# Performance work log

Measured on AMD Instinct MI355X. Metric: run time of the kernel, lower is better.

Reference implementation:

```python
import jax, jax.numpy as jnp
import numpy as np

VOCAB = 1024   # must equal HID (embedding Linear consumes vocab-sized x)
HID = 1024
EMB = 256
NOS = 12
B, M = 512, 8
TEMP = 1.0


def setup_inputs() -> dict:
    key = jax.random.key(0)
    ks = jax.random.split(key, 12)
    N = B * M
    target = jax.random.normal(ks[0], (B, M, HID), jnp.float32)
    # precomputed standard Gumbel noise per step (training=True path)
    u = jax.random.uniform(ks[1], (NOS, N, VOCAB), jnp.float32, 1e-6, 1.0 - 1e-6)
    gumbels = -jnp.log(-jnp.log(u))
    sh = 1.0 / np.sqrt(HID)
    sv = 1.0 / np.sqrt(VOCAB)
    sos = 0.01 * jax.random.normal(ks[2], (EMB,), jnp.float32)
    W_ih = jax.random.uniform(ks[3], (HID, EMB), jnp.float32, -sh, sh)
    b_ih = jax.random.uniform(ks[4], (HID,), jnp.float32, -sh, sh)
    W_hh = jax.random.uniform(ks[5], (HID, HID), jnp.float32, -sh, sh)
    b_hh = jax.random.uniform(ks[6], (HID,), jnp.float32, -sh, sh)
    W_out = jax.random.uniform(ks[7], (VOCAB, HID), jnp.float32, -sh, sh)
    b_out = jax.random.uniform(ks[8], (VOCAB,), jnp.float32, -sh, sh)
    W_emb = jax.random.uniform(ks[9], (EMB, VOCAB), jnp.float32, -sv, sv)
    b_emb = jax.random.uniform(ks[10], (EMB,), jnp.float32, -sv, sv)
    return dict(target=target, gumbels=gumbels, sos=sos,
                W_ih=W_ih, b_ih=b_ih, W_hh=W_hh, b_hh=b_hh,
                W_out=W_out, b_out=b_out, W_emb=W_emb, b_emb=b_emb)


def reference(target, gumbels, sos, W_ih, b_ih, W_hh, b_hh, W_out, b_out, W_emb, b_emb):
    b_, m_, h_ = target.shape
    prev = target.reshape(b_ * m_, h_)            # [N, HID]
    e0 = jnp.broadcast_to(sos, (prev.shape[0], sos.shape[0]))  # [N, EMB]

    def step(carry, g):
        prev_h, e = carry
        h = jnp.tanh(e @ W_ih.T + b_ih + prev_h @ W_hh.T + b_hh)   # RNNCell
        logits = h @ W_out.T + b_out                               # [N, VOCAB]
        x = jax.nn.softmax((logits + g) / TEMP, axis=-1)           # gumbel-softmax
        e_next = x @ W_emb.T + b_emb                               # [N, EMB]
        return (h, e_next), x

    _, xs = jax.lax.scan(step, (prev, e0), gumbels)  # xs: [NOS, N, VOCAB]
    return jnp.transpose(xs, (1, 0, 2))              # [N, NOS, VOCAB]
```

## Files before the change

kernel.cpp:

```cpp
#include <hip/hip_runtime.h>

#define N_TOT 4096
#define HIDN  1024
#define EMBD  256
#define VOC   1024
#define NSTEP 12

typedef __bf16 bf16;
typedef _Float16 h16;
typedef __bf16 bf16x8 __attribute__((ext_vector_type(8)));
typedef __bf16 bf16x4 __attribute__((ext_vector_type(4)));
typedef _Float16 h16x8 __attribute__((ext_vector_type(8)));
typedef float  f32x4  __attribute__((ext_vector_type(4)));

#define VMCNT(n) asm volatile("s_waitcnt vmcnt(" #n ")" ::: "memory")
#define MEMFENCE() asm volatile("" ::: "memory")

static __device__ __forceinline__ f32x4 mfma16(bf16x8 a, bf16x8 b, f32x4 c) {
  return __builtin_amdgcn_mfma_f32_16x16x32_bf16(a, b, c, 0, 0, 0);
}

static __device__ __forceinline__ void gload16(const bf16* g, bf16* l) {
  __builtin_amdgcn_global_load_lds(
      (const __attribute__((address_space(1))) void*)g,
      (__attribute__((address_space(3))) void*)l, 16, 0, 0);
}


__global__ void prep_kernel(const float* __restrict__ Wih, const float* __restrict__ Whh,
                            const float* __restrict__ Wout, const float* __restrict__ Wemb,
                            const float* __restrict__ target, const float* __restrict__ sos,
                            const float* __restrict__ bih, const float* __restrict__ bhh,
                            bf16* __restrict__ wih_b, bf16* __restrict__ whh_b,
                            bf16* __restrict__ wout_b, bf16* __restrict__ wemb_b,
                            bf16* __restrict__ hbuf, bf16* __restrict__ ebuf,
                            float* __restrict__ bias1) {
  for (int q = blockIdx.x * blockDim.x + threadIdx.x; q < 1966336;
       q += blockDim.x * gridDim.x) {
    if (q < 1703936) {
      const float* s; bf16* d; int o;
      if (q < 65536)        { s = Wih;    d = wih_b;  o = q; }
      else if (q < 327680)  { s = Whh;    d = whh_b;  o = q - 65536; }
      else if (q < 589824)  { s = Wout;   d = wout_b; o = q - 327680; }
      else if (q < 655360)  { s = Wemb;   d = wemb_b; o = q - 589824; }
      else                  { s = target; d = hbuf;   o = q - 655360; }
      f32x4 v = *(const f32x4*)&s[(size_t)o * 4];
      bf16x4 b; b[0] = (bf16)v.x; b[1] = (bf16)v.y; b[2] = (bf16)v.z; b[3] = (bf16)v.w;
      *(bf16x4*)&d[(size_t)o * 4] = b;
    } else if (q < 1966080) {
      int o = q - 1703936;
      f32x4 v = *(const f32x4*)&sos[(o & 63) * 4];
      bf16x4 b; b[0] = (bf16)v.x; b[1] = (bf16)v.y; b[2] = (bf16)v.z; b[3] = (bf16)v.w;
      *(bf16x4*)&ebuf[(size_t)o * 4] = b;
    } else {
      int o = q - 1966080;
      f32x4 a = *(const f32x4*)&bih[o * 4];
      f32x4 c = *(const f32x4*)&bhh[o * 4];
      f32x4 r; r.x = a.x + c.x; r.y = a.y + c.y; r.z = a.z + c.z; r.w = a.w + c.w;
      *(f32x4*)&bias1[o * 4] = r;
    }
  }
}


template <bool TWO, int NT>
static __device__ __forceinline__ void pipe_gemm(
    const bf16* __restrict__ A0, const bf16* __restrict__ B0, int K0,
    const bf16* __restrict__ A1, const bf16* __restrict__ B1, int K1,
    bf16* lds, int m0, int n0, int w, int lane, f32x4 acc[4][2])
{
  const int wr = w >> 1, wc = w & 1;
  const int lr = lane & 15, lk = lane >> 4;
  const int srow = lane >> 3;
  const int scol = (((lane & 7) ^ srow) << 3);

  auto stage = [&](int t, int bsel) {
    const bf16 *A, *B; int K, k0;
    if (TWO && t < 4) { A = A0; B = B0; K = K0; k0 = t << 6; }
    else if (TWO)     { A = A1; B = B1; K = K1; k0 = (t - 4) << 6; }
    else              { A = A0; B = B0; K = K0; k0 = t << 6; }
    bf16* base = lds + bsel * 12288;
#pragma unroll
    for (int r = 0; r < 4; ++r)
      gload16(&A[(size_t)(m0 + w * 32 + r * 8 + srow) * K + k0 + scol],
              base + (w * 32 + r * 8) * 64);
#pragma unroll
    for (int r = 0; r < 2; ++r)
      gload16(&B[(size_t)(n0 + w * 16 + r * 8 + srow) * K + k0 + scol],
              base + 8192 + (w * 16 + r * 8) * 64);
  };

  stage(0, 0); stage(1, 1);
  VMCNT(6);
  MEMFENCE();
  __builtin_amdgcn_s_barrier();
  MEMFENCE();
  for (int t = 0; t < NT; ++t) {
    if (t + 2 < NT) stage(t + 2, (t + 2) % 3);
    const bf16* Ab = lds + (t % 3) * 12288;
    const bf16* Bb = Ab + 8192;
#pragma unroll
    for (int kk = 0; kk < 2; ++kk) {
      bf16x8 af[4], bfr[2];
#pragma unroll
      for (int mi = 0; mi < 4; ++mi) {
        int row = wr * 64 + mi * 16 + lr;
        af[mi] = *(const bf16x8*)&Ab[row * 64 + ((((kk << 2) | lk) ^ (row & 7)) << 3)];
      }
#pragma unroll
      for (int ni = 0; ni < 2; ++ni) {
        int row = wc * 32 + ni * 16 + lr;
        bfr[ni] = *(const bf16x8*)&Bb[row * 64 + ((((kk << 2) | lk) ^ (row & 7)) << 3)];
      }
#pragma unroll
      for (int mi = 0; mi < 4; ++mi)
#pragma unroll
        for (int ni = 0; ni < 2; ++ni)
          acc[mi][ni] = mfma16(af[mi], bfr[ni], acc[mi][ni]);
    }
    if (t < NT - 2)       VMCNT(6);
    else if (t == NT - 2) VMCNT(0);
    MEMFENCE();
    __builtin_amdgcn_s_barrier();
    MEMFENCE();
  }
}


__global__ __launch_bounds__(256, 2)
void rnn_cell_kernel(const bf16* __restrict__ e,
                     const bf16* __restrict__ hprev,
                     const bf16* __restrict__ Wih,
                     const bf16* __restrict__ Whh,
                     const float* __restrict__ bias,
                     bf16* __restrict__ hnew)
{
  __shared__ bf16 lds[3 * 12288];
  const int tid = threadIdx.x;
  const int lane = tid & 63;
  const int w = tid >> 6;
  const int wr = w >> 1, wc = w & 1;
  const int id = (blockIdx.x & 7) * 64 + (blockIdx.x >> 3);
  const int m0 = (id >> 4) * 128;
  const int n0 = (id & 15) * 64;
  const int lr = lane & 15, lk = lane >> 4;

  f32x4 acc[4][2] = {};
  pipe_gemm<true, 20>(e, Wih, EMBD, hprev, Whh, HIDN, lds, m0, n0, w, lane, acc);

#pragma unroll
  for (int mi = 0; mi < 4; ++mi) {
    int rowb = m0 + wr * 64 + mi * 16 + lk * 4;
#pragma unroll
    for (int ni = 0; ni < 2; ++ni) {
      int col = n0 + wc * 32 + ni * 16 + lr;
      float bs = bias[col];
#pragma unroll
      for (int j = 0; j < 4; ++j)
        hnew[(size_t)(rowb + j) * HIDN + col] = (bf16)tanhf(acc[mi][ni][j] + bs);
    }
  }
}


__global__ __launch_bounds__(256, 2)
void logits_kernel(const bf16* __restrict__ h,
                   const bf16* __restrict__ Wout,
                   const float* __restrict__ bout,
                   h16* __restrict__ lbuf)
{
  __shared__ bf16 lds[3 * 12288];
  const int tid = threadIdx.x;
  const int lane = tid & 63;
  const int w = tid >> 6;
  const int wr = w >> 1, wc = w & 1;
  const int id = (blockIdx.x & 7) * 64 + (blockIdx.x >> 3);
  const int m0 = (id >> 4) * 128;
  const int n0 = (id & 15) * 64;
  const int lr = lane & 15, lk = lane >> 4;

  f32x4 acc[4][2] = {};
  pipe_gemm<false, 16>(h, Wout, HIDN, nullptr, nullptr, 0, lds, m0, n0, w, lane, acc);

#pragma unroll
  for (int mi = 0; mi < 4; ++mi) {
    int rowb = m0 + wr * 64 + mi * 16 + lk * 4;
#pragma unroll
    for (int ni = 0; ni < 2; ++ni) {
      int col = n0 + wc * 32 + ni * 16 + lr;
      float bs = bout[col];
#pragma unroll
      for (int j = 0; j < 4; ++j) {
        int row = rowb + j;
        lbuf[(size_t)row * VOC + col] = (h16)(acc[mi][ni][j] + bs);
      }
    }
  }
}


__global__ __launch_bounds__(512)
void softmax_emb_kernel(const h16* __restrict__ lbuf,
                        const float* __restrict__ gum,
                        const bf16* __restrict__ Wemb,
                        const float* __restrict__ bemb,
                        float* __restrict__ out,
                        bf16* __restrict__ enext,
                        int step)
{
  __shared__ bf16 xs[16 * 1032];
  const int tid = threadIdx.x;
  const int lane = tid & 63;
  const int w = tid >> 6;
  const int n0 = blockIdx.x * 16;

  for (int rr = 0; rr < 2; ++rr) {
    int r = w + rr * 8;
    const h16* lrow = lbuf + (size_t)(n0 + r) * VOC;
    const float* grow = gum + (size_t)(n0 + r) * VOC;
    float s[16];
    float m = -1e30f;
#pragma unroll
    for (int i = 0; i < 2; ++i) {
      h16x8 lv = *(const h16x8*)&lrow[i * 512 + lane * 8];
      f32x4 g0 = *(const f32x4*)&grow[i * 512 + lane * 8];
      f32x4 g1 = *(const f32x4*)&grow[i * 512 + lane * 8 + 4];
#pragma unroll
      for (int j = 0; j < 4; ++j) {
        float f0 = (float)lv[j] + g0[j];
        float f1 = (float)lv[4 + j] + g1[j];
        s[i * 8 + j] = f0; s[i * 8 + 4 + j] = f1;
        m = fmaxf(m, fmaxf(f0, f1));
      }
    }
#pragma unroll
    for (int off = 32; off; off >>= 1) m = fmaxf(m, __shfl_xor(m, off));
    float sum = 0.f;
#pragma unroll
    for (int i = 0; i < 16; ++i) { s[i] = __expf(s[i] - m); sum += s[i]; }
#pragma unroll
    for (int off = 32; off; off >>= 1) sum += __shfl_xor(sum, off);
    float inv = 1.0f / sum;
    float* orow = out + ((size_t)(n0 + r) * NSTEP + step) * VOC;
#pragma unroll
    for (int i = 0; i < 2; ++i) {
      f32x4 v0, v1;
      bf16x8 bv;
#pragma unroll
      for (int j = 0; j < 4; ++j) {
        float x0 = s[i * 8 + j] * inv;
        float x1 = s[i * 8 + 4 + j] * inv;
        v0[j] = x0; v1[j] = x1;
        bv[j] = (bf16)x0; bv[4 + j] = (bf16)x1;
      }
      *(f32x4*)&orow[i * 512 + lane * 8] = v0;
      *(f32x4*)&orow[i * 512 + lane * 8 + 4] = v1;
      *(bf16x8*)&xs[r * 1032 + i * 512 + lane * 8] = bv;
    }
  }
  __syncthreads();

  const int lr = lane & 15, lk = lane >> 4;
  f32x4 acc[2] = {};
  for (int k0 = 0; k0 < VOC; k0 += 32) {
    bf16x8 a = *(bf16x8*)&xs[lr * 1032 + k0 + lk * 8];
#pragma unroll
    for (int ni = 0; ni < 2; ++ni) {
      int col = w * 32 + ni * 16 + lr;
      bf16x8 b = *(const bf16x8*)&Wemb[(size_t)col * VOC + k0 + lk * 8];
      acc[ni] = mfma16(a, b, acc[ni]);
    }
  }
#pragma unroll
  for (int ni = 0; ni < 2; ++ni) {
    int col = w * 32 + ni * 16 + lr;
    float bb = bemb[col];
#pragma unroll
    for (int j = 0; j < 4; ++j) {
      int n = n0 + lk * 4 + j;
      enext[(size_t)n * EMBD + col] = (bf16)(acc[ni][j] + bb);
    }
  }
}


extern "C" void kernel_launch(void* const* d_in, const int* in_sizes, int n_in,
                              void* d_out, int out_size, void* d_ws, size_t ws_size,
                              hipStream_t stream) {
  const float* target  = (const float*)d_in[0];
  const float* gumbels = (const float*)d_in[1];
  const float* sos     = (const float*)d_in[2];
  const float* W_ih    = (const float*)d_in[3];
  const float* b_ih    = (const float*)d_in[4];
  const float* W_hh    = (const float*)d_in[5];
  const float* b_hh    = (const float*)d_in[6];
  const float* W_out   = (const float*)d_in[7];
  const float* b_out   = (const float*)d_in[8];
  const float* W_emb   = (const float*)d_in[9];
  const float* b_emb   = (const float*)d_in[10];
  float* out = (float*)d_out;

  char* ws = (char*)d_ws;
  bf16* wih_b  = (bf16*)(ws);
  bf16* whh_b  = (bf16*)(ws + (1u << 20));
  bf16* wout_b = (bf16*)(ws + (3u << 20));
  bf16* wemb_b = (bf16*)(ws + (5u << 20));
  float* bias1 = (float*)(ws + (6u << 20));
  bf16* hbuf0  = (bf16*)(ws + (7u << 20));
  bf16* hbuf1  = (bf16*)(ws + (15u << 20));
  bf16* ebuf   = (bf16*)(ws + (23u << 20));
  h16*  lbuf   = (h16*) (ws + (25u << 20));

  prep_kernel<<<2048, 256, 0, stream>>>(W_ih, W_hh, W_out, W_emb, target, sos,
                                        b_ih, b_hh, wih_b, whh_b, wout_b, wemb_b,
                                        hbuf0, ebuf, bias1);

  bf16* hb[2] = {hbuf0, hbuf1};
  for (int t = 0; t < NSTEP; ++t) {
    bf16* hp = hb[t & 1];
    bf16* hn = hb[(t + 1) & 1];
    rnn_cell_kernel<<<(N_TOT / 128) * (HIDN / 64), 256, 0, stream>>>(
        ebuf, hp, wih_b, whh_b, bias1, hn);
    logits_kernel<<<(N_TOT / 128) * (VOC / 64), 256, 0, stream>>>(
        hn, wout_b, b_out, lbuf);
    softmax_emb_kernel<<<N_TOT / 16, 512, 0, stream>>>(
        lbuf, gumbels + (size_t)t * N_TOT * VOC, wemb_b, b_emb, out, ebuf, t);
  }
}
```

Baseline: 657.8 us.

## Use 2-wave blocks with 64x64 warp tiles, double buffering, and fast tanh

The two GEMM kernels now run 128-thread blocks where each wave computes a 64x64 output tile (4x4 MFMA fragments) instead of 4 waves at 64x32. The LDS pipeline drops from triple to double buffering, with one stage prefetched and a full vmcnt(0) wait every iteration. tanhf is replaced by an exp-based fast_tanh. The aim is more register-level reuse of A and B fragments and cheaper activation math, at the cost of fewer waves per block, a shallower prefetch depth, and more stalls waiting on global loads.

```diff
diff --git a/kernel.cpp b/kernel.cpp
--- a/kernel.cpp
+++ b/kernel.cpp
@@ -18,6 +18,11 @@
 
 static __device__ __forceinline__ f32x4 mfma16(bf16x8 a, bf16x8 b, f32x4 c) {
   return __builtin_amdgcn_mfma_f32_16x16x32_bf16(a, b, c, 0, 0, 0);
+}
+
+static __device__ __forceinline__ float fast_tanh(float x) {
+  float e = __expf(2.0f * x);
+  return 1.0f - 2.0f / (e + 1.0f);
 }
 
 static __device__ __forceinline__ void gload16(const bf16* g, bf16* l) {
@@ -67,9 +72,8 @@
 static __device__ __forceinline__ void pipe_gemm(
     const bf16* __restrict__ A0, const bf16* __restrict__ B0, int K0,
     const bf16* __restrict__ A1, const bf16* __restrict__ B1, int K1,
-    bf16* lds, int m0, int n0, int w, int lane, f32x4 acc[4][2])
+    bf16* lds, int m0, int n0, int w, int lane, f32x4 acc[4][4])
 {
-  const int wr = w >> 1, wc = w & 1;
   const int lr = lane & 15, lk = lane >> 4;
   const int srow = lane >> 3;
   const int scol = (((lane & 7) ^ srow) << 3);
@@ -81,53 +85,54 @@
     else              { A = A0; B = B0; K = K0; k0 = t << 6; }
     bf16* base = lds + bsel * 12288;
 #pragma unroll
+    for (int r = 0; r < 8; ++r)
+      gload16(&A[(size_t)(m0 + w * 64 + r * 8 + srow) * K + k0 + scol],
+              base + (w * 64 + r * 8) * 64);
+#pragma unroll
     for (int r = 0; r < 4; ++r)
-      gload16(&A[(size_t)(m0 + w * 32 + r * 8 + srow) * K + k0 + scol],
-              base + (w * 32 + r * 8) * 64);
-#pragma unroll
-    for (int r = 0; r < 2; ++r)
-      gload16(&B[(size_t)(n0 + w * 16 + r * 8 + srow) * K + k0 + scol],
-              base + 8192 + (w * 16 + r * 8) * 64);
+      gload16(&B[(size_t)(n0 + w * 32 + r * 8 + srow) * K + k0 + scol],
+              base + 8192 + (w * 32 + r * 8) * 64);
   };
 
-  stage(0, 0); stage(1, 1);
-  VMCNT(6);
+  stage(0, 0);
+  VMCNT(0);
   MEMFENCE();
   __builtin_amdgcn_s_barrier();
   MEMFENCE();
   for (int t = 0; t < NT; ++t) {
-    if (t + 2 < NT) stage(t + 2, (t + 2) % 3);
-    const bf16* Ab = lds + (t % 3) * 12288;
+    if (t + 1 < NT) stage(t + 1, (t + 1) & 1);
+    const bf16* Ab = lds + (t & 1) * 12288;
     const bf16* Bb = Ab + 8192;
 #pragma unroll
     for (int kk = 0; kk < 2; ++kk) {
-      bf16x8 af[4], bfr[2];
+      bf16x8 af[4], bf[4];
 #pragma unroll
       for (int mi = 0; mi < 4; ++mi) {
-        int row = wr * 64 + mi * 16 + lr;
+        int row = w * 64 + mi * 16 + lr;
         af[mi] = *(const bf16x8*)&Ab[row * 64 + ((((kk << 2) | lk) ^ (row & 7)) << 3)];
       }
 #pragma unroll
-      for (int ni = 0; ni < 2; ++ni) {
-        int row = wc * 32 + ni * 16 + lr;
-        bfr[ni] = *(const bf16x8*)&Bb[row * 64 + ((((kk << 2) | lk) ^ (row & 7)) << 3)];
+      for (int ni = 0; ni < 4; ++ni) {
+        int row = ni * 16 + lr;
+        bf[ni] = *(const bf16x8*)&Bb[row * 64 + ((((kk << 2) | lk) ^ (row & 7)) << 3)];
       }
 #pragma unroll
       for (int mi = 0; mi < 4; ++mi)
 #pragma unroll
-        for (int ni = 0; ni < 2; ++ni)
-          acc[mi][ni] = mfma16(af[mi], bfr[ni], acc[mi][ni]);
-    }
-    if (t < NT - 2)       VMCNT(6);
-    else if (t == NT - 2) VMCNT(0);
-    MEMFENCE();
-    __builtin_amdgcn_s_barrier();
-    MEMFENCE();
-  }
-}
-
-
-__global__ __launch_bounds__(256, 2)
+        for (int ni = 0; ni < 4; ++ni)
+          acc[mi][ni] = mfma16(af[mi], bf[ni], acc[mi][ni]);
+    }
+    if (t + 1 < NT) {
+      VMCNT(0);
+      MEMFENCE();
+      __builtin_amdgcn_s_barrier();
+      MEMFENCE();
+    }
+  }
+}
+
+
+__global__ __launch_bounds__(128)
 void rnn_cell_kernel(const bf16* __restrict__ e,
                      const bf16* __restrict__ hprev,
                      const bf16* __restrict__ Wih,
@@ -135,59 +140,57 @@
                      const float* __restrict__ bias,
                      bf16* __restrict__ hnew)
 {
-  __shared__ bf16 lds[3 * 12288];
+  __shared__ bf16 lds[2 * 12288];
   const int tid = threadIdx.x;
   const int lane = tid & 63;
   const int w = tid >> 6;
-  const int wr = w >> 1, wc = w & 1;
   const int id = (blockIdx.x & 7) * 64 + (blockIdx.x >> 3);
   const int m0 = (id >> 4) * 128;
   const int n0 = (id & 15) * 64;
   const int lr = lane & 15, lk = lane >> 4;
 
-  f32x4 acc[4][2] = {};
+  f32x4 acc[4][4] = {};
   pipe_gemm<true, 20>(e, Wih, EMBD, hprev, Whh, HIDN, lds, m0, n0, w, lane, acc);
 
 #pragma unroll
   for (int mi = 0; mi < 4; ++mi) {
-    int rowb = m0 + wr * 64 + mi * 16 + lk * 4;
-#pragma unroll
-    for (int ni = 0; ni < 2; ++ni) {
-      int col = n0 + wc * 32 + ni * 16 + lr;
+    int rowb = m0 + w * 64 + mi * 16 + lk * 4;
+#pragma unroll
+    for (int ni = 0; ni < 4; ++ni) {
+      int col = n0 + ni * 16 + lr;
       float bs = bias[col];
 #pragma unroll
       for (int j = 0; j < 4; ++j)
-        hnew[(size_t)(rowb + j) * HIDN + col] = (bf16)tanhf(acc[mi][ni][j] + bs);
-    }
-  }
-}
-
-
-__global__ __launch_bounds__(256, 2)
+        hnew[(size_t)(rowb + j) * HIDN + col] = (bf16)fast_tanh(acc[mi][ni][j] + bs);
+    }
+  }
+}
+
+
+__global__ __launch_bounds__(128)
 void logits_kernel(const bf16* __restrict__ h,
                    const bf16* __restrict__ Wout,
                    const float* __restrict__ bout,
                    h16* __restrict__ lbuf)
 {
-  __shared__ bf16 lds[3 * 12288];
+  __shared__ bf16 lds[2 * 12288];
   const int tid = threadIdx.x;
   const int lane = tid & 63;
   const int w = tid >> 6;
-  const int wr = w >> 1, wc = w & 1;
   const int id = (blockIdx.x & 7) * 64 + (blockIdx.x >> 3);
   const int m0 = (id >> 4) * 128;
   const int n0 = (id & 15) * 64;
   const int lr = lane & 15, lk = lane >> 4;
 
-  f32x4 acc[4][2] = {};
+  f32x4 acc[4][4] = {};
   pipe_gemm<false, 16>(h, Wout, HIDN, nullptr, nullptr, 0, lds, m0, n0, w, lane, acc);
 
 #pragma unroll
   for (int mi = 0; mi < 4; ++mi) {
-    int rowb = m0 + wr * 64 + mi * 16 + lk * 4;
-#pragma unroll
-    for (int ni = 0; ni < 2; ++ni) {
-      int col = n0 + wc * 32 + ni * 16 + lr;
+    int rowb = m0 + w * 64 + mi * 16 + lk * 4;
+#pragma unroll
+    for (int ni = 0; ni < 4; ++ni) {
+      int col = n0 + ni * 16 + lr;
       float bs = bout[col];
 #pragma unroll
       for (int j = 0; j < 4; ++j) {
@@ -319,9 +322,9 @@
   for (int t = 0; t < NSTEP; ++t) {
     bf16* hp = hb[t & 1];
     bf16* hn = hb[(t + 1) & 1];
-    rnn_cell_kernel<<<(N_TOT / 128) * (HIDN / 64), 256, 0, stream>>>(
+    rnn_cell_kernel<<<(N_TOT / 128) * (HIDN / 64), 128, 0, stream>>>(
         ebuf, hp, wih_b, whh_b, bias1, hn);
-    logits_kernel<<<(N_TOT / 128) * (VOC / 64), 256, 0, stream>>>(
+    logits_kernel<<<(N_TOT / 128) * (VOC / 64), 128, 0, stream>>>(
         hn, wout_b, b_out, lbuf);
     softmax_emb_kernel<<<N_TOT / 16, 512, 0, stream>>>(
         lbuf, gumbels + (size_t)t * N_TOT * VOC, wemb_b, b_emb, out, ebuf, t);
```

Result: slower. 780.7 us (+18.7%).
